# Performance work log

Hardware: AMD Instinct MI355X
Metric: run time of the kernel (lower is better)

## Reference

```python
import jax, jax.numpy as jnp
import numpy as np

K_PERIODS = 4
PMAX = 64
MIN_PERIOD = 8


def setup_inputs() -> dict:
    key = jax.random.key(0)
    x = jax.random.normal(key, (32, 512, 64), dtype=jnp.float32)  # [B, T, N]
    return {"x": x}


def reference(x):
    """Dense, fixed-shape equivalent of PeriodicityTransform.forward (mask=None).

    Instead of a Python list of variable-shape PeriodGroup tiles, returns a
    padded tensor values[bn, k, c, p] where for each (sequence bn, freq rank k)
    with period P and cycles C, values[bn, k, :C, :P] equals the torch tile
    seqs[bn, T-C*P : T].reshape(C, P); entries outside (C, P) are zero.
    Also returns the integer periods and cycles per (bn, k).
    """
    B, T, N = x.shape
    BN = B * N
    seqs = jnp.transpose(x, (0, 2, 1)).reshape(BN, T)  # [BN, T]

    # top-k nonzero FFT frequencies (DC bin zeroed out)
    spec = jnp.fft.rfft(seqs, axis=-1)
    mag2 = spec.real ** 2 + spec.imag ** 2
    mag2 = mag2.at[..., 0].set(0.0)
    _, kidx = jax.lax.top_k(mag2, K_PERIODS)  # [BN, K]
    kidx = jnp.maximum(kidx, 1)

    # periods = clamp(T // f, min=MIN_PERIOD, max=PMAX); cycles = T // period
    periods = jnp.clip(T // kidx, MIN_PERIOD, PMAX)  # [BN, K]
    cycles = T // periods                              # [BN, K]

    cmax = T // MIN_PERIOD  # static upper bound on cycles
    i = jnp.arange(cmax)[:, None]   # cycle index  [Cmax, 1]
    j = jnp.arange(PMAX)[None, :]   # phase index  [1, Pmax]

    start = T - cycles * periods                                   # [BN, K]
    idx = start[..., None, None] + i * periods[..., None, None] + j  # [BN,K,Cmax,Pmax]
    idx = jnp.clip(idx, 0, T - 1)
    valid = (i < cycles[..., None, None]) & (j < periods[..., None, None])

    gathered = jnp.take_along_axis(
        seqs[:, None, :], idx.reshape(BN, K_PERIODS, -1), axis=-1
    ).reshape(BN, K_PERIODS, cmax, PMAX)
    values = jnp.where(valid, gathered, jnp.float32(0.0))
    return values, periods, cycles
```

## Files before the change

kernel.cpp:

```cpp
#include <hip/hip_runtime.h>
#include <math.h>

#define TT 512
#define KP 4

typedef unsigned long long u64;

#define SYNCL() asm volatile("s_waitcnt lgkmcnt(0)\n\ts_barrier" ::: "memory")
#define SYNCW() do { asm volatile("s_waitcnt lgkmcnt(0)" ::: "memory"); \
                     __builtin_amdgcn_sched_barrier(0); } while (0)

__global__ __launch_bounds__(256) void periodicity_kernel(const float* __restrict__ x,
                                                          float* __restrict__ out) {
    const int bn   = (blockIdx.x & 7) * 256 + (blockIdx.x >> 3);
    const int tid  = threadIdx.x;
    const int lane = tid & 63;
    const int wid  = tid >> 6;
    const int b = bn >> 6;
    const int n = bn & 63;

    __shared__ float2 tw[TT];
    __shared__ __align__(16) float row[TT];
    __shared__ __align__(16) float2 buf[TT];
    __shared__ __align__(16) u64 keys[256];
    __shared__ double candV8[8];

    float sv, cv;
    sincosf((float)(2.0 * M_PI / 512.0) * (float)tid, &sv, &cv);
    tw[tid]       = make_float2(cv, -sv);
    tw[tid + 256] = make_float2(-cv, sv);

    const float* xb = x + (size_t)b * (TT * 64) + n;
    {
        float v0 = xb[(size_t)tid * 64];
        float v1 = xb[(size_t)(tid + 256) * 64];
        row[tid] = v0;  row[tid + 256] = v1;
        float sum = v0 + v1, dif = v0 - v1;
        buf[tid]       = make_float2(sum, 0.f);
        buf[tid + 256] = make_float2(dif * cv, -dif * sv);
    }
    SYNCL();

    if (wid < 2) {
        const int h = wid;
        float2* bb = &buf[h << 8];

        #pragma unroll
        for (int stg = 0; stg < 3; ++stg) {
            const int Q  = 64 >> (2 * stg);
            const int g  = lane >> (6 - 2 * stg);
            const int i  = lane & (Q - 1);
            const int base = g * (Q << 2) + i;
            float2 x0 = bb[base],         x1 = bb[base + Q];
            float2 x2 = bb[base + 2 * Q], x3 = bb[base + 3 * Q];
            float2 A  = make_float2(x0.x + x2.x, x0.y + x2.y);
            float2 Bm = make_float2(x0.x - x2.x, x0.y - x2.y);
            float2 Cc = make_float2(x1.x + x3.x, x1.y + x3.y);
            float2 D  = make_float2(x1.x - x3.x, x1.y - x3.y);
            float2 y0 = make_float2(A.x + Cc.x, A.y + Cc.y);
            float2 y2 = make_float2(A.x - Cc.x, A.y - Cc.y);
            float2 y1 = make_float2(Bm.x + D.y, Bm.y - D.x);
            float2 y3 = make_float2(Bm.x - D.y, Bm.y + D.x);
            const int m = i << (1 + 2 * stg);
            float2 t1 = tw[m], t2 = tw[2 * m], t3 = tw[3 * m];
            bb[base]         = y0;
            bb[base + Q]     = make_float2(y1.x * t1.x - y1.y * t1.y, y1.x * t1.y + y1.y * t1.x);
            bb[base + 2 * Q] = make_float2(y2.x * t2.x - y2.y * t2.y, y2.x * t2.y + y2.y * t2.x);
            bb[base + 3 * Q] = make_float2(y3.x * t3.x - y3.y * t3.y, y3.x * t3.y + y3.y * t3.x);
            SYNCW();
        }

        {
            const int g = lane;
            const int base = g << 2;
            float2 x0 = bb[base],     x1 = bb[base + 1];
            float2 x2 = bb[base + 2], x3 = bb[base + 3];
            float2 A  = make_float2(x0.x + x2.x, x0.y + x2.y);
            float2 Bm = make_float2(x0.x - x2.x, x0.y - x2.y);
            float2 Cc = make_float2(x1.x + x3.x, x1.y + x3.y);
            float2 D  = make_float2(x1.x - x3.x, x1.y - x3.y);
            float2 y0 = make_float2(A.x + Cc.x, A.y + Cc.y);
            float2 y2 = make_float2(A.x - Cc.x, A.y - Cc.y);
            float2 y1 = make_float2(Bm.x + D.y, Bm.y - D.x);
            float2 y3 = make_float2(Bm.x - D.y, Bm.y + D.x);
            const int revg = ((g & 3) << 4) | (((g >> 2) & 3) << 2) | ((g >> 4) & 3);
            const int f0 = 2 * revg + h;
            float m0 = y0.x * y0.x + y0.y * y0.y;
            float m1 = y1.x * y1.x + y1.y * y1.y;
            float m2 = y2.x * y2.x + y2.y * y2.y;
            float m3 = y3.x * y3.x + y3.y * y3.y;
            u64 kA, kB;
            if (f0 == 0) {
                kA = ((u64)__float_as_uint(m1) << 32) | (u64)(256 - 128);
                kB = ((u64)__float_as_uint(m2) << 32) | (u64)(256 - 256);
            } else {
                kA = ((u64)__float_as_uint(m0) << 32) | (u64)(256 - f0);
                kB = ((u64)__float_as_uint(m1) << 32) | (u64)(256 - (f0 + 128));
            }
            ulonglong2* kv = (ulonglong2*)keys;
            kv[(h << 6) + g] = make_ulonglong2(kA, kB);
        }
    }
    SYNCL();

    int   fbin[8];
    float cmag[8];
    {
        const ulonglong2* kv = (const ulonglong2*)keys;
        ulonglong2 p0v = kv[lane * 2];
        ulonglong2 p1v = kv[lane * 2 + 1];
        u64 k0 = p0v.x, k1 = p0v.y, k2 = p1v.x, k3 = p1v.y;
        #define CSWAP(a, b) { if (a < b) { u64 _t = a; a = b; b = _t; } }
        CSWAP(k0, k1) CSWAP(k2, k3) CSWAP(k0, k2) CSWAP(k1, k3) CSWAP(k1, k2)
        #undef CSWAP
        #pragma unroll
        for (int r = 0; r < 8; ++r) {
            u64 w = k0;
            #pragma unroll
            for (int off = 32; off >= 1; off >>= 1) {
                u64 o = __shfl_xor(w, off);
                if (o > w) w = o;
            }
            if (k0 == w) { k0 = k1; k1 = k2; k2 = k3; k3 = 0; }
            fbin[r] = 256 - (int)(w & 0xff);
            cmag[r] = __uint_as_float((unsigned)(w >> 32));
        }
    }

    int per[KP], cycv[KP], stv[KP];
    {
        const bool needRefine =
            ((cmag[0] - cmag[1]) <= 1e-4f * cmag[0]) || ((cmag[1] - cmag[2]) <= 1e-4f * cmag[1]) ||
            ((cmag[2] - cmag[3]) <= 1e-4f * cmag[2]) || ((cmag[3] - cmag[4]) <= 1e-4f * cmag[3]);
        int bins[KP];
        if (!needRefine) {
            #pragma unroll
            for (int k = 0; k < KP; ++k) bins[k] = fbin[k];
        } else {
            {
                const int cid = tid >> 5;
                const int sub = tid & 31;
                int fc;
                switch (cid) {
                    case 0: fc = fbin[0]; break;
                    case 1: fc = fbin[1]; break;
                    case 2: fc = fbin[2]; break;
                    case 3: fc = fbin[3]; break;
                    case 4: fc = fbin[4]; break;
                    case 5: fc = fbin[5]; break;
                    case 6: fc = fbin[6]; break;
                    default: fc = fbin[7]; break;
                }
                const int t0 = sub * 16;
                const double W = 6.2831853071795864769 / 512.0;
                double zr, zi, wr, wi;
                sincos(W * (double)((fc * t0) & 511), &zi, &zr);
                sincos(W * (double)fc, &wi, &wr);
                double ar = 0.0, ai = 0.0;
                const float4* r4 = (const float4*)row;
                #pragma unroll
                for (int v4i = 0; v4i < 4; ++v4i) {
                    float4 xv = r4[sub * 4 + v4i];
                    #define STEP(comp)                                   \
                        { double xd = (double)xv.comp;                   \
                          ar = fma(xd, zr, ar); ai = fma(xd, zi, ai);    \
                          double tq = zr * wr - zi * wi;                 \
                          zi = fma(zr, wi, zi * wr); zr = tq; }
                    STEP(x) STEP(y) STEP(z) STEP(w)
                    #undef STEP
                }
                #pragma unroll
                for (int off = 16; off >= 1; off >>= 1) {
                    ar += __shfl_xor(ar, off);
                    ai += __shfl_xor(ai, off);
                }
                if (sub == 0) candV8[cid] = ar * ar + ai * ai;
            }
            SYNCL();
            unsigned chosen = 0;
            #pragma unroll
            for (int k = 0; k < KP; ++k) {
                double bv = -1.0; int bbin = 0x7fffffff; int bj = 0;
                #pragma unroll
                for (int j = 0; j < 8; ++j) {
                    if (chosen & (1u << j)) continue;
                    double vj = candV8[j];
                    int    bjn = fbin[j];
                    if (vj > bv || (vj == bv && bjn < bbin)) { bv = vj; bbin = bjn; bj = j; }
                }
                chosen |= (1u << bj);
                bins[k] = bbin;
            }
        }
        #pragma unroll
        for (int k = 0; k < KP; ++k) {
            int p = TT / bins[k];
            p = p < 8 ? 8 : (p > 64 ? 64 : p);
            per[k]  = p;
            cycv[k] = TT / p;
            stv[k]  = TT - cycv[k] * p;
        }
    }

    const size_t VOFF = (size_t)2048 * KP * 64 * 64;
    if (tid == 0) {
        #pragma unroll
        for (int k = 0; k < KP; ++k) {
            out[VOFF + (size_t)bn * KP + k]        = (float)per[k];
            out[VOFF + 8192 + (size_t)bn * KP + k] = (float)cycv[k];
        }
    }

    float* outv = out + (size_t)bn * (KP * 64 * 64);
    const int c_local = tid >> 4;
    const int p0 = (tid & 15) << 2;
    #pragma unroll
    for (int it = 0; it < 16; ++it) {
        const int k = it >> 2;
        const int c = ((it & 3) << 4) + c_local;
        float4 v = make_float4(0.f, 0.f, 0.f, 0.f);
        const int P = per[k], C = cycv[k], S0 = stv[k];
        if (c < C) {
            const int base = S0 + c * P;
            if (p0 + 3 < P) {
                v.x = row[base + p0];
                v.y = row[base + p0 + 1];
                v.z = row[base + p0 + 2];
                v.w = row[base + p0 + 3];
            } else {
                if (p0     < P) v.x = row[base + p0];
                if (p0 + 1 < P) v.y = row[base + p0 + 1];
                if (p0 + 2 < P) v.z = row[base + p0 + 2];
                if (p0 + 3 < P) v.w = row[base + p0 + 3];
            }
        }
        *(float4*)(outv + (size_t)it * 1024 + (size_t)tid * 4) = v;
    }
}

extern "C" void kernel_launch(void* const* d_in, const int* in_sizes, int n_in,
                              void* d_out, int out_size, void* d_ws, size_t ws_size,
                              hipStream_t stream) {
    const float* x = (const float*)d_in[0];
    float* out = (float*)d_out;
    hipLaunchKernelGGL(periodicity_kernel, dim3(2048), dim3(256), 0, stream, x, out);
}
```

Baseline: 30.48 us.

## Zero-fill provably-empty output regions early in idle waves during FFT

Uses the two waves that sit idle during the FFT stages to write zeros to output tile regions that are zero for every possible period (columns beyond max width for a cycle index). The final gather-store loop then writes only the potentially non-zero column ranges. This overlaps part of the large output store traffic with FFT compute. It relies on the bound that a cycle index c implies period at most 512/(c+1), and it changes the store access pattern.

```diff
diff --git a/kernel.cpp b/kernel.cpp
--- a/kernel.cpp
+++ b/kernel.cpp
@@ -25,13 +25,15 @@
     __shared__ __align__(16) u64 keys[256];
     __shared__ double candV8[8];
 
+    float* outv = out + (size_t)bn * (KP * 64 * 64);
+
     float sv, cv;
     sincosf((float)(2.0 * M_PI / 512.0) * (float)tid, &sv, &cv);
     tw[tid]       = make_float2(cv, -sv);
     tw[tid + 256] = make_float2(-cv, sv);
 
-    const float* xb = x + (size_t)b * (TT * 64) + n;
-    {
+    {
+        const float* xb = x + (size_t)b * (TT * 64) + n;
         float v0 = xb[(size_t)tid * 64];
         float v1 = xb[(size_t)(tid + 256) * 64];
         row[tid] = v0;  row[tid + 256] = v1;
@@ -88,7 +90,6 @@
             float m0 = y0.x * y0.x + y0.y * y0.y;
             float m1 = y1.x * y1.x + y1.y * y1.y;
             float m2 = y2.x * y2.x + y2.y * y2.y;
-            float m3 = y3.x * y3.x + y3.y * y3.y;
             u64 kA, kB;
             if (f0 == 0) {
                 kA = ((u64)__float_as_uint(m1) << 32) | (u64)(256 - 128);
@@ -97,8 +98,23 @@
                 kA = ((u64)__float_as_uint(m0) << 32) | (u64)(256 - f0);
                 kB = ((u64)__float_as_uint(m1) << 32) | (u64)(256 - (f0 + 128));
             }
-            ulonglong2* kv = (ulonglong2*)keys;
-            kv[(h << 6) + g] = make_ulonglong2(kA, kB);
+            ((ulonglong2*)keys)[(h << 6) + g] = make_ulonglong2(kA, kB);
+        }
+    } else {
+        const int tg = tid - 128;
+        const int j  = tg & 15;
+        const int cb = tg >> 4;
+        const float4 z = make_float4(0.f, 0.f, 0.f, 0.f);
+        #pragma unroll
+        for (int c0 = 8; c0 < 64; c0 += 8) {
+            const int c = c0 + cb;
+            const int W = max(8, 512 / (c + 1));
+            const int W4c = (W + 3) >> 2;
+            if (j >= W4c) {
+                #pragma unroll
+                for (int k = 0; k < KP; ++k)
+                    *(float4*)(outv + k * 4096 + c * 64 + j * 4) = z;
+            }
         }
     }
     SYNCL();
@@ -211,30 +227,38 @@
         }
     }
 
-    float* outv = out + (size_t)bn * (KP * 64 * 64);
-    const int c_local = tid >> 4;
-    const int p0 = (tid & 15) << 2;
-    #pragma unroll
-    for (int it = 0; it < 16; ++it) {
-        const int k = it >> 2;
-        const int c = ((it & 3) << 4) + c_local;
-        float4 v = make_float4(0.f, 0.f, 0.f, 0.f);
-        const int P = per[k], C = cycv[k], S0 = stv[k];
-        if (c < C) {
-            const int base = S0 + c * P;
-            if (p0 + 3 < P) {
-                v.x = row[base + p0];
-                v.y = row[base + p0 + 1];
-                v.z = row[base + p0 + 2];
-                v.w = row[base + p0 + 3];
-            } else {
-                if (p0     < P) v.x = row[base + p0];
-                if (p0 + 1 < P) v.y = row[base + p0 + 1];
-                if (p0 + 2 < P) v.z = row[base + p0 + 2];
-                if (p0 + 3 < P) v.w = row[base + p0 + 3];
-            }
-        }
-        *(float4*)(outv + (size_t)it * 1024 + (size_t)tid * 4) = v;
+    {
+        const int cr = tid >> 4;
+        const int j  = tid & 15;
+        #pragma unroll
+        for (int cg = 0; cg < 4; ++cg) {
+            const int c = cg * 16 + cr;
+            const int W = min(64, max(8, 512 / (c + 1)));
+            const int W4c = (W + 3) >> 2;
+            if (j < W4c) {
+                const int p0 = j << 2;
+                #pragma unroll
+                for (int k = 0; k < KP; ++k) {
+                    const int P = per[k], C = cycv[k], S0 = stv[k];
+                    float4 v = make_float4(0.f, 0.f, 0.f, 0.f);
+                    if (c < C) {
+                        const int base = S0 + c * P;
+                        if (p0 + 3 < P) {
+                            v.x = row[base + p0];
+                            v.y = row[base + p0 + 1];
+                            v.z = row[base + p0 + 2];
+                            v.w = row[base + p0 + 3];
+                        } else {
+                            if (p0     < P) v.x = row[base + p0];
+                            if (p0 + 1 < P) v.y = row[base + p0 + 1];
+                            if (p0 + 2 < P) v.z = row[base + p0 + 2];
+                            if (p0 + 3 < P) v.w = row[base + p0 + 3];
+                        }
+                    }
+                    *(float4*)(outv + k * 4096 + c * 64 + p0) = v;
+                }
+            }
+        }
     }
 }
 
```

Result: slower. 34.53 us (+13.3%).
